# Optimization experiments

Hardware: AMD Instinct MI355X
Metric: run time of the kernel (lower is better)

## Reference

```python
import math
import jax, jax.numpy as jnp
import numpy as np

D_MODEL = 1024
HEADS = 16
D_K = D_MODEL // HEADS
BATCH = 4
SEQ = 2048


def setup_inputs() -> dict:
    key = jax.random.key(0)
    ks = jax.random.split(key, 7)
    q = jax.random.normal(ks[0], (BATCH, SEQ, D_MODEL), dtype=jnp.float32)
    k = jax.random.normal(ks[1], (BATCH, SEQ, D_MODEL), dtype=jnp.float32)
    v = jax.random.normal(ks[2], (BATCH, SEQ, D_MODEL), dtype=jnp.float32)
    # causal mask: True = masked (filled with -inf), broadcastable over batch & heads
    mask = jnp.triu(jnp.ones((SEQ, SEQ), dtype=bool), k=1)[None, None, :, :]
    s = 1.0 / math.sqrt(D_MODEL)
    Wq = jax.random.normal(ks[3], (D_MODEL, D_MODEL), dtype=jnp.float32) * s
    Wk = jax.random.normal(ks[4], (D_MODEL, D_MODEL), dtype=jnp.float32) * s
    Wv = jax.random.normal(ks[5], (D_MODEL, D_MODEL), dtype=jnp.float32) * s
    Wo = jax.random.normal(ks[6], (D_MODEL, D_MODEL), dtype=jnp.float32) * s
    return {"q": q, "k": k, "v": v, "mask": mask, "Wq": Wq, "Wk": Wk, "Wv": Wv, "Wo": Wo}


def reference(q, k, v, mask, Wq, Wk, Wv, Wo):
    B, S, _ = q.shape
    # Linear(d_model, d_model, bias=False): y = x @ W.T
    def proj(x, W):
        return (x @ W.T).reshape(B, S, HEADS, D_K).transpose(0, 2, 1, 3)  # [B,H,S,Dk]
    qh, kh, vh = proj(q, Wq), proj(k, Wk), proj(v, Wv)
    scores = jnp.einsum('bhqd,bhkd->bhqk', qh, kh) / math.sqrt(D_K)
    scores = jnp.where(mask, -jnp.inf, scores)
    attn = jax.nn.softmax(scores, axis=-1)  # dropout p=0 is identity
    ctx = jnp.einsum('bhqk,bhkd->bhqd', attn, vh)
    ctx = ctx.transpose(0, 2, 1, 3).reshape(B, S, D_MODEL)
    return ctx @ Wo.T
```

## Files before the change

kernel.cpp:

```cpp
#include <hip/hip_runtime.h>
#include <hip/hip_bf16.h>
#include <stdint.h>

#define S_LEN 2048
#define DMODEL 1024
#define HEADS 16
#define DK 64
#define LDK 72

#define QSCALE 0.18033688011112042f

typedef __attribute__((ext_vector_type(8))) short bf16x8;
typedef __attribute__((ext_vector_type(4))) float f32x4;

__device__ __forceinline__ unsigned short f2bf(float f) {
    union { float f; unsigned u; } c; c.f = f;
    unsigned u = c.u;
    u += 0x7fffu + ((u >> 16) & 1u);
    return (unsigned short)(u >> 16);
}

__device__ __forceinline__ unsigned pkbf(float a, float b) {
    union { float f; unsigned u; } ca, cb; ca.f = a; cb.f = b;
    unsigned ua = ca.u + (0x7fffu + ((ca.u >> 16) & 1u));
    unsigned ub = cb.u + (0x7fffu + ((cb.u >> 16) & 1u));
    return __builtin_amdgcn_perm(ub, ua, 0x07060302);
}

__device__ __forceinline__ unsigned cvtpk(float a, float b) {
    unsigned r;
    asm("v_cvt_pk_bf16_f32 %0, %1, %2" : "=v"(r) : "v"(a), "v"(b));
    return r;
}

__device__ __forceinline__ void g2lds16(const unsigned short* g, unsigned short* l) {
    __builtin_amdgcn_global_load_lds((const __attribute__((address_space(1))) void*)g,
                                     (__attribute__((address_space(3))) void*)l, 16, 0, 0);
}

__global__ __launch_bounds__(256) void convert_kernel(
    const float* __restrict__ q, const float* __restrict__ k, const float* __restrict__ v,
    const float* __restrict__ Wq, const float* __restrict__ Wk, const float* __restrict__ Wv,
    const float* __restrict__ Wo,
    unsigned short* __restrict__ qbf, unsigned short* __restrict__ kbf,
    unsigned short* __restrict__ vbf, unsigned short* __restrict__ wbf)
{
    const float* src; unsigned short* dst; int n8;
    const int y = blockIdx.y;
    if (y == 0)      { src = q;  dst = qbf;           n8 = 1048576; }
    else if (y == 1) { src = k;  dst = kbf;           n8 = 1048576; }
    else if (y == 2) { src = v;  dst = vbf;           n8 = 1048576; }
    else if (y == 3) { src = Wq; dst = wbf;           n8 = 131072; }
    else if (y == 4) { src = Wk; dst = wbf + 1048576; n8 = 131072; }
    else if (y == 5) { src = Wv; dst = wbf + 2097152; n8 = 131072; }
    else             { src = Wo; dst = wbf + 3145728; n8 = 131072; }
    int i = blockIdx.x * 256 + threadIdx.x;
    if (i >= n8) return;
    float4 f0 = ((const float4*)src)[(size_t)2 * i];
    float4 f1 = ((const float4*)src)[(size_t)2 * i + 1];
    union { unsigned u[4]; uint4 v; } o;
    o.u[0] = pkbf(f0.x, f0.y); o.u[1] = pkbf(f0.z, f0.w);
    o.u[2] = pkbf(f1.x, f1.y); o.u[3] = pkbf(f1.z, f1.w);
    *(uint4*)&dst[(size_t)8 * i] = o.v;
}

__device__ __forceinline__ void gemm_core_128x128(
    const unsigned short* __restrict__ Apanel,
    const unsigned short* __restrict__ Bpanel,
    unsigned short* sm,
    f32x4 acc[4][4])
{
    const int t    = threadIdx.x;
    const int lane = t & 63;
    const int w    = t >> 6;
    const int wm   = w >> 1;
    const int wn   = w & 1;
    const int lrow = lane & 15;
    const int quad = lane >> 4;

    const int l8   = lane >> 3;
    const int c16s = (lane & 7) ^ l8;
    const unsigned short* gA = Apanel + (size_t)(w * 8 + l8) * 1024 + c16s * 8;
    const unsigned short* gB = Bpanel + (size_t)(w * 8 + l8) * 1024 + c16s * 8;
    unsigned short* lA = sm + w * 512;
    unsigned short* lB = sm + 8192 + w * 512;

#define STAGE_KT(bufsel, kt) do {                                         \
        unsigned short* la = lA + (bufsel) * 16384;                       \
        unsigned short* lb = lB + (bufsel) * 16384;                       \
        const unsigned short* ga = gA + (kt) * 64;                        \
        const unsigned short* gb = gB + (kt) * 64;                        \
        g2lds16(ga,                       la);                            \
        g2lds16(ga + (size_t)32 * 1024,   la + 2048);                     \
        g2lds16(ga + (size_t)64 * 1024,   la + 4096);                     \
        g2lds16(ga + (size_t)96 * 1024,   la + 6144);                     \
        g2lds16(gb,                       lb);                            \
        g2lds16(gb + (size_t)32 * 1024,   lb + 2048);                     \
        g2lds16(gb + (size_t)64 * 1024,   lb + 4096);                     \
        g2lds16(gb + (size_t)96 * 1024,   lb + 6144);                     \
    } while (0)

    for (int i = 0; i < 4; i++) for (int j = 0; j < 4; j++) acc[i][j] = (f32x4){0.f, 0.f, 0.f, 0.f};

    STAGE_KT(0, 0);

#pragma unroll 1
    for (int kt = 0; kt < 16; ++kt) {
        const int buf = kt & 1;
        if (kt < 15) {
            STAGE_KT(buf ^ 1, kt + 1);
            asm volatile("s_waitcnt vmcnt(8)" ::: "memory");
        } else {
            asm volatile("s_waitcnt vmcnt(0)" ::: "memory");
        }
        __builtin_amdgcn_sched_barrier(0);
        __builtin_amdgcn_s_barrier();
        __builtin_amdgcn_sched_barrier(0);

        const unsigned short* tA = sm + buf * 16384;
        const unsigned short* tB = sm + buf * 16384 + 8192;
        for (int kh = 0; kh < 2; ++kh) {
            const int cs = ((kh * 4 + quad) ^ (lrow & 7)) * 8;
            bf16x8 a[4], b[4];
            for (int mi = 0; mi < 4; mi++)
                a[mi] = *(const bf16x8*)&tA[(wm * 64 + mi * 16 + lrow) * 64 + cs];
            for (int nj = 0; nj < 4; nj++)
                b[nj] = *(const bf16x8*)&tB[(wn * 64 + nj * 16 + lrow) * 64 + cs];
            __builtin_amdgcn_s_setprio(1);
            for (int mi = 0; mi < 4; mi++)
                for (int nj = 0; nj < 4; nj++)
                    acc[mi][nj] = __builtin_amdgcn_mfma_f32_16x16x32_bf16(a[mi], b[nj], acc[mi][nj], 0, 0, 0);
            __builtin_amdgcn_s_setprio(0);
        }
        __builtin_amdgcn_sched_barrier(0);
        __builtin_amdgcn_s_barrier();
        __builtin_amdgcn_sched_barrier(0);
    }
#undef STAGE_KT
}

__global__ __launch_bounds__(256, 2) void proj_gemm_kernel(
    const unsigned short* __restrict__ qbf, const unsigned short* __restrict__ kbf,
    const unsigned short* __restrict__ vbf, const unsigned short* __restrict__ wbf,
    unsigned short* __restrict__ qh, unsigned short* __restrict__ kh,
    unsigned short* __restrict__ vh_t)
{
    const int h   = (int)(blockIdx.x + 64 * (blockIdx.y + 8 * blockIdx.z));
    const int s   = h >> 3;
    const int panel = (h & 7) * 24 + (s >> 3);
    const int by  = s & 7;
    const int z   = panel >> 6;
    const int bx  = panel & 63;

    const unsigned short* A; const unsigned short* Bm; unsigned short* Y;
    if (z == 0)      { A = qbf; Bm = wbf;           Y = qh;   }
    else if (z == 1) { A = kbf; Bm = wbf + 1048576; Y = kh;   }
    else             { A = vbf; Bm = wbf + 2097152; Y = vh_t; }

    __shared__ unsigned short sm[32768];

    const int m0 = bx * 128;
    const int n0 = by * 128;

    f32x4 acc[4][4];
    gemm_core_128x128(A + (size_t)m0 * 1024, Bm + (size_t)n0 * 1024, sm, acc);

    const int t = threadIdx.x, lane = t & 63;
    const int wm = (t >> 6) >> 1, wn = (t >> 6) & 1;
    const int lrow = lane & 15, quad = lane >> 4;
    const float scale = (z == 0) ? QSCALE : 1.0f;
    for (int i = 0; i < 4; i++) {
        int grow = m0 + wm * 64 + i * 16 + quad * 4;
        for (int j = 0; j < 4; j++) {
            int gcol = n0 + wn * 64 + j * 16 + lrow;
            int hh = gcol >> 6, d = gcol & 63;
            for (int r = 0; r < 4; r++) {
                int row = grow + r;
                int b_ = row >> 11;
                int s_ = row & 2047;
                unsigned short val = f2bf(acc[i][j][r] * scale);
                if (z == 2)
                    Y[(((size_t)(b_ * HEADS + hh) * DK) + d) * S_LEN + s_] = val;
                else
                    Y[(((size_t)(b_ * HEADS + hh) * S_LEN) + s_) * DK + d] = val;
            }
        }
    }
}

__global__ __launch_bounds__(256, 2) void outproj_gemm_kernel(
    const unsigned short* __restrict__ ctx, const unsigned short* __restrict__ wobf,
    float* __restrict__ out)
{
    const int h   = (int)(blockIdx.x + 64 * blockIdx.y);
    const int s   = h >> 3;
    const int bx  = (h & 7) * 8 + (s >> 3);
    const int by  = s & 7;

    __shared__ unsigned short sm[32768];

    const int m0 = bx * 128;
    const int n0 = by * 128;

    f32x4 acc[4][4];
    gemm_core_128x128(ctx + (size_t)m0 * 1024, wobf + (size_t)n0 * 1024, sm, acc);

    const int t = threadIdx.x, lane = t & 63;
    const int wm = (t >> 6) >> 1, wn = (t >> 6) & 1;
    const int lrow = lane & 15, quad = lane >> 4;
    for (int i = 0; i < 4; i++) {
        int grow = m0 + wm * 64 + i * 16 + quad * 4;
        for (int j = 0; j < 4; j++) {
            int gcol = n0 + wn * 64 + j * 16 + lrow;
            for (int r = 0; r < 4; r++)
                out[(size_t)(grow + r) * DMODEL + gcol] = acc[i][j][r];
        }
    }
}

__global__ __launch_bounds__(256, 4) void attn_kernel(
    const unsigned short* __restrict__ qh, const unsigned short* __restrict__ kh,
    const unsigned short* __restrict__ vh_t, unsigned short* __restrict__ ctx)
{
    __shared__ unsigned short sK[64 * LDK];
    __shared__ unsigned short sVt[64 * LDK];
    __shared__ unsigned short sPT[4][16 * LDK];

    const int t    = threadIdx.x;
    const int lane = t & 63;
    const int wid  = t >> 6;
    const int lin  = (int)(blockIdx.y * gridDim.x + blockIdx.x);
    const int wlin = (lin & 7) * 128 + (lin >> 3);
    const int qx   = wlin & 15;
    const int bh   = wlin >> 4;
    const size_t base = (size_t)bh * S_LEN * DK;
    const int lrow = lane & 15;
    const int quad = lane >> 4;
    const int b_ = bh >> 4, h_ = bh & 15;
    unsigned short* myPT = &sPT[wid][0];

    const int sr0 = t >> 3;
    const int sc0 = (t & 7) * 8;
    const unsigned short* gK = kh + base;
    const unsigned short* gV = vh_t + base;

    for (int pass = 0; pass < 2; ++pass) {
        const int qt = pass ? (31 - qx) : qx;
        const int q0 = qt * 64;
        const int qw0 = q0 + wid * 16;

        bf16x8 qreg[2];
        for (int h = 0; h < 2; ++h)
            qreg[h] = *(const bf16x8*)&qh[base + (size_t)(qw0 + lrow) * DK + h * 32 + quad * 8];

        f32x4 o[4];
        for (int mf = 0; mf < 4; mf++) o[mf] = (f32x4){0.f, 0.f, 0.f, 0.f};
        float lstat = 0.f;

        const int ntiles = qt + 1;

        uint4 rK0 = *(const uint4*)&gK[(size_t)sr0 * DK + sc0];
        uint4 rK1 = *(const uint4*)&gK[(size_t)(sr0 + 32) * DK + sc0];
        uint4 rV0 = *(const uint4*)&gV[(size_t)sr0 * S_LEN + sc0];
        uint4 rV1 = *(const uint4*)&gV[(size_t)(sr0 + 32) * S_LEN + sc0];

        for (int kt = 0; kt < ntiles; ++kt) {
            const int k0 = kt * 64;
            __syncthreads();
            *(uint4*)&sK [sr0 * LDK + sc0]        = rK0;
            *(uint4*)&sK [(sr0 + 32) * LDK + sc0] = rK1;
            *(uint4*)&sVt[sr0 * LDK + sc0]        = rV0;
            *(uint4*)&sVt[(sr0 + 32) * LDK + sc0] = rV1;
            if (kt + 1 < ntiles) {
                const int kn = k0 + 64;
                rK0 = *(const uint4*)&gK[(size_t)(kn + sr0) * DK + sc0];
                rK1 = *(const uint4*)&gK[(size_t)(kn + sr0 + 32) * DK + sc0];
                rV0 = *(const uint4*)&gV[(size_t)sr0 * S_LEN + kn + sc0];
                rV1 = *(const uint4*)&gV[(size_t)(sr0 + 32) * S_LEN + kn + sc0];
            }
            __syncthreads();

            f32x4 st[4];
            for (int mf = 0; mf < 4; mf++) st[mf] = (f32x4){0.f, 0.f, 0.f, 0.f};
            for (int h = 0; h < 2; ++h) {
                bf16x8 kf[4];
                for (int mf = 0; mf < 4; mf++)
                    kf[mf] = *(const bf16x8*)&sK[(mf * 16 + lrow) * LDK + h * 32 + quad * 8];
                __builtin_amdgcn_s_setprio(1);
                for (int mf = 0; mf < 4; mf++)
                    st[mf] = __builtin_amdgcn_mfma_f32_16x16x32_bf16(kf[mf], qreg[h], st[mf], 0, 0, 0);
                __builtin_amdgcn_s_setprio(0);
            }

            if (kt == qt) {
                const int qidx = qw0 + lrow;
                for (int mf = 0; mf < 4; mf++)
                    for (int r = 0; r < 4; r++) {
                        int key = k0 + mf * 16 + quad * 4 + r;
                        if (key > qidx) st[mf][r] = -INFINITY;
                    }
            }

            {
                float rsum = 0.f;
                for (int mf = 0; mf < 4; mf++) {
                    float p0 = exp2f(st[mf][0]);
                    float p1 = exp2f(st[mf][1]);
                    float p2 = exp2f(st[mf][2]);
                    float p3 = exp2f(st[mf][3]);
                    rsum += (p0 + p1) + (p2 + p3);
                    uint2 pk;
                    pk.x = cvtpk(p0, p1);
                    pk.y = cvtpk(p2, p3);
                    *(uint2*)&myPT[lrow * LDK + mf * 16 + quad * 4] = pk;
                }
                lstat += rsum;
            }

            for (int h = 0; h < 2; ++h) {
                bf16x8 vf[4];
                for (int mf = 0; mf < 4; mf++)
                    vf[mf] = *(const bf16x8*)&sVt[(mf * 16 + lrow) * LDK + h * 32 + quad * 8];
                bf16x8 pf = *(const bf16x8*)&myPT[lrow * LDK + h * 32 + quad * 8];
                __builtin_amdgcn_s_setprio(1);
                for (int mf = 0; mf < 4; mf++)
                    o[mf] = __builtin_amdgcn_mfma_f32_16x16x32_bf16(vf[mf], pf, o[mf], 0, 0, 0);
                __builtin_amdgcn_s_setprio(0);
            }
        }

        {
            float ls = lstat;
            ls += __shfl_xor(ls, 16);
            ls += __shfl_xor(ls, 32);
            float inv = 1.f / ls;
            int s_ = qw0 + lrow;
            size_t rowbase = (((size_t)(b_ * S_LEN + s_)) * HEADS + h_) * DK;
            for (int mf = 0; mf < 4; mf++) {
                int d0 = mf * 16 + quad * 4;
                uint2 pk;
                pk.x = pkbf(o[mf][0] * inv, o[mf][1] * inv);
                pk.y = pkbf(o[mf][2] * inv, o[mf][3] * inv);
                *(uint2*)&ctx[rowbase + d0] = pk;
            }
        }
    }
}

__global__ __launch_bounds__(256) void proj_fb_kernel(
    const float* __restrict__ q, const float* __restrict__ k, const float* __restrict__ v,
    const float* __restrict__ Wq, const float* __restrict__ Wk, const float* __restrict__ Wv,
    unsigned short* __restrict__ qh, unsigned short* __restrict__ kh, unsigned short* __restrict__ vh_t)
{
    const float* X; const float* W; unsigned short* Y;
    if (blockIdx.z == 0)      { X = q; W = Wq; Y = qh; }
    else if (blockIdx.z == 1) { X = k; W = Wk; Y = kh; }
    else                      { X = v; W = Wv; Y = vh_t; }

    __shared__ short sA[128 * LDK];
    __shared__ short sB[128 * LDK];
    const int t = threadIdx.x, lane = t & 63, wid = t >> 6;
    const int wrow = (wid >> 1) * 64, wcol = (wid & 1) * 64;
    const int m0 = blockIdx.x * 128, n0 = blockIdx.y * 128;
    const int lrow = lane & 15, quad = lane >> 4, lk = quad * 8;

    f32x4 acc[4][4];
    for (int i = 0; i < 4; i++) for (int j = 0; j < 4; j++) acc[i][j] = (f32x4){0.f, 0.f, 0.f, 0.f};

    for (int kb = 0; kb < DMODEL; kb += 64) {
        for (int it = 0; it < 8; ++it) {
            int idx = t + it * 256;
            int row = idx >> 4, c4 = (idx & 15) * 4;
            float4 fa = *(const float4*)&X[(size_t)(m0 + row) * DMODEL + kb + c4];
            float4 fb = *(const float4*)&W[(size_t)(n0 + row) * DMODEL + kb + c4];
            short4 sa = { (short)f2bf(fa.x), (short)f2bf(fa.y), (short)f2bf(fa.z), (short)f2bf(fa.w) };
            short4 sb = { (short)f2bf(fb.x), (short)f2bf(fb.y), (short)f2bf(fb.z), (short)f2bf(fb.w) };
            *(short4*)&sA[row * LDK + c4] = sa;
            *(short4*)&sB[row * LDK + c4] = sb;
        }
        __syncthreads();
        for (int kk = 0; kk < 64; kk += 32) {
            bf16x8 a[4], b[4];
            for (int i = 0; i < 4; i++) a[i] = *(const bf16x8*)&sA[(wrow + i * 16 + lrow) * LDK + kk + lk];
            for (int j = 0; j < 4; j++) b[j] = *(const bf16x8*)&sB[(wcol + j * 16 + lrow) * LDK + kk + lk];
            for (int i = 0; i < 4; i++)
                for (int j = 0; j < 4; j++)
                    acc[i][j] = __builtin_amdgcn_mfma_f32_16x16x32_bf16(a[i], b[j], acc[i][j], 0, 0, 0);
        }
        __syncthreads();
    }

    const float scale = (blockIdx.z == 0) ? QSCALE : 1.0f;
    for (int i = 0; i < 4; i++) {
        int grow = m0 + wrow + i * 16 + quad * 4;
        for (int j = 0; j < 4; j++) {
            int gcol = n0 + wcol + j * 16 + lrow;
            int h = gcol >> 6, d = gcol & 63;
            for (int r = 0; r < 4; r++) {
                int row = grow + r, b_ = row >> 11, s_ = row & 2047;
                unsigned short val = f2bf(acc[i][j][r] * scale);
                if (blockIdx.z == 2)
                    Y[(((size_t)(b_ * HEADS + h) * DK) + d) * S_LEN + s_] = val;
                else
                    Y[(((size_t)(b_ * HEADS + h) * S_LEN) + s_) * DK + d] = val;
            }
        }
    }
}

__global__ __launch_bounds__(256) void outproj_fb_kernel(
    const unsigned short* __restrict__ ctx, const float* __restrict__ Wo, float* __restrict__ out)
{
    __shared__ short sA[128 * LDK];
    __shared__ short sB[128 * LDK];
    const int t = threadIdx.x, lane = t & 63, wid = t >> 6;
    const int wrow = (wid >> 1) * 64, wcol = (wid & 1) * 64;
    const int m0 = blockIdx.x * 128, n0 = blockIdx.y * 128;
    const int lrow = lane & 15, quad = lane >> 4, lk = quad * 8;

    f32x4 acc[4][4];
    for (int i = 0; i < 4; i++) for (int j = 0; j < 4; j++) acc[i][j] = (f32x4){0.f, 0.f, 0.f, 0.f};

    for (int kb = 0; kb < DMODEL; kb += 64) {
        for (int it = 0; it < 4; ++it) {
            int idx = t + it * 256;
            int row = idx >> 3, c8 = (idx & 7) * 8;
            *(uint4*)&sA[row * LDK + c8] = *(const uint4*)&ctx[(size_t)(m0 + row) * DMODEL + kb + c8];
        }
        for (int it = 0; it < 8; ++it) {
            int idx = t + it * 256;
            int row = idx >> 4, c4 = (idx & 15) * 4;
            float4 fb = *(const float4*)&Wo[(size_t)(n0 + row) * DMODEL + kb + c4];
            short4 sb = { (short)f2bf(fb.x), (short)f2bf(fb.y), (short)f2bf(fb.z), (short)f2bf(fb.w) };
            *(short4*)&sB[row * LDK + c4] = sb;
        }
        __syncthreads();
        for (int kk = 0; kk < 64; kk += 32) {
            bf16x8 a[4], b[4];
            for (int i = 0; i < 4; i++) a[i] = *(const bf16x8*)&sA[(wrow + i * 16 + lrow) * LDK + kk + lk];
            for (int j = 0; j < 4; j++) b[j] = *(const bf16x8*)&sB[(wcol + j * 16 + lrow) * LDK + kk + lk];
            for (int i = 0; i < 4; i++)
                for (int j = 0; j < 4; j++)
                    acc[i][j] = __builtin_amdgcn_mfma_f32_16x16x32_bf16(a[i], b[j], acc[i][j], 0, 0, 0);
        }
        __syncthreads();
    }

    for (int i = 0; i < 4; i++) {
        int grow = m0 + wrow + i * 16 + quad * 4;
        for (int j = 0; j < 4; j++) {
            int gcol = n0 + wcol + j * 16 + lrow;
            for (int r = 0; r < 4; r++)
                out[(size_t)(grow + r) * DMODEL + gcol] = acc[i][j][r];
        }
    }
}

extern "C" void kernel_launch(void* const* d_in, const int* in_sizes, int n_in,
                              void* d_out, int out_size, void* d_ws, size_t ws_size,
                              hipStream_t stream)
{
    const float* q  = (const float*)d_in[0];
    const float* k  = (const float*)d_in[1];
    const float* v  = (const float*)d_in[2];
    const float* Wq = (const float*)d_in[4];
    const float* Wk = (const float*)d_in[5];
    const float* Wv = (const float*)d_in[6];
    const float* Wo = (const float*)d_in[7];
    float* out = (float*)d_out;

    const size_t M8 = (size_t)8 * 1024 * 1024;
    const size_t need = (size_t)(52) * 1024 * 1024 * 2;

    if (ws_size >= need) {
        unsigned short* qbf  = (unsigned short*)d_ws;
        unsigned short* kbf  = qbf + M8;
        unsigned short* vbf  = kbf + M8;
        unsigned short* wbf  = vbf + M8;
        unsigned short* qh   = wbf + (size_t)4 * 1024 * 1024;
        unsigned short* kh   = qh + M8;
        unsigned short* vh_t = kh + M8;
        unsigned short* ctx  = qbf;

        dim3 gCvt(4096, 7);
        convert_kernel<<<gCvt, 256, 0, stream>>>(q, k, v, Wq, Wk, Wv, Wo, qbf, kbf, vbf, wbf);

        dim3 gProj(64, 8, 3);
        proj_gemm_kernel<<<gProj, 256, 0, stream>>>(qbf, kbf, vbf, wbf, qh, kh, vh_t);

        dim3 gAttn(16, 64);
        attn_kernel<<<gAttn, 256, 0, stream>>>(qh, kh, vh_t, ctx);

        dim3 gOut(64, 8);
        outproj_gemm_kernel<<<gOut, 256, 0, stream>>>(ctx, wbf + (size_t)3 * 1024 * 1024, out);
    } else {
        unsigned short* qh   = (unsigned short*)d_ws;
        unsigned short* kh   = qh + M8;
        unsigned short* vh_t = kh + M8;
        unsigned short* ctx  = vh_t + M8;

        dim3 gProj(64, 8, 3);
        proj_fb_kernel<<<gProj, 256, 0, stream>>>(q, k, v, Wq, Wk, Wv, qh, kh, vh_t);

        dim3 gAttn(16, 64);
        attn_kernel<<<gAttn, 256, 0, stream>>>(qh, kh, vh_t, ctx);

        dim3 gOut(64, 8);
        outproj_fb_kernel<<<gOut, 256, 0, stream>>>(ctx, Wo, out);
    }
}
```

Before: 329.0 us.

## Store GEMM operands in tiled 128x64 blocked layout for contiguous panel loads

The bf16 conversion kernel and the attention ctx writer now emit operands in a blocked layout where each 128-row by 64-column k-tile is contiguous. The GEMM core then loads each k-step from one contiguous 16 KB block instead of 128 rows strided by 1024 elements, and the fallback out-projection reads ctx with the same layout. This aims to improve DRAM/TLB locality and reduce address arithmetic for the staged global-to-LDS loads. Every producer and consumer of these buffers has to agree on the layout, so a missed fallback path would produce wrong results.

Measured after the change: 339.1 us. 3.1% more time.

```diff
diff --git a/kernel.cpp b/kernel.cpp
--- a/kernel.cpp
+++ b/kernel.cpp
@@ -9,6 +9,7 @@
 #define LDK 72
 
 #define QSCALE 0.18033688011112042f
+
 
 typedef __attribute__((ext_vector_type(8))) short bf16x8;
 typedef __attribute__((ext_vector_type(4))) float f32x4;
@@ -61,7 +62,10 @@
     union { unsigned u[4]; uint4 v; } o;
     o.u[0] = pkbf(f0.x, f0.y); o.u[1] = pkbf(f0.z, f0.w);
     o.u[2] = pkbf(f1.x, f1.y); o.u[3] = pkbf(f1.z, f1.w);
-    *(uint4*)&dst[(size_t)8 * i] = o.v;
+    const int m  = i >> 7;
+    const int k8 = (i & 127) * 8;
+    const size_t didx = ((size_t)((m >> 7) * 16 + (k8 >> 6)) * 128 + (m & 127)) * 64 + (k8 & 63);
+    *(uint4*)&dst[didx] = o.v;
 }
 
 __device__ __forceinline__ void gemm_core_128x128(
@@ -80,24 +84,24 @@
 
     const int l8   = lane >> 3;
     const int c16s = (lane & 7) ^ l8;
-    const unsigned short* gA = Apanel + (size_t)(w * 8 + l8) * 1024 + c16s * 8;
-    const unsigned short* gB = Bpanel + (size_t)(w * 8 + l8) * 1024 + c16s * 8;
+    const unsigned short* gA = Apanel + (w * 8 + l8) * 64 + c16s * 8;
+    const unsigned short* gB = Bpanel + (w * 8 + l8) * 64 + c16s * 8;
     unsigned short* lA = sm + w * 512;
     unsigned short* lB = sm + 8192 + w * 512;
 
 #define STAGE_KT(bufsel, kt) do {                                         \
         unsigned short* la = lA + (bufsel) * 16384;                       \
         unsigned short* lb = lB + (bufsel) * 16384;                       \
-        const unsigned short* ga = gA + (kt) * 64;                        \
-        const unsigned short* gb = gB + (kt) * 64;                        \
-        g2lds16(ga,                       la);                            \
-        g2lds16(ga + (size_t)32 * 1024,   la + 2048);                     \
-        g2lds16(ga + (size_t)64 * 1024,   la + 4096);                     \
-        g2lds16(ga + (size_t)96 * 1024,   la + 6144);                     \
-        g2lds16(gb,                       lb);                            \
-        g2lds16(gb + (size_t)32 * 1024,   lb + 2048);                     \
-        g2lds16(gb + (size_t)64 * 1024,   lb + 4096);                     \
-        g2lds16(gb + (size_t)96 * 1024,   lb + 6144);                     \
+        const unsigned short* ga = gA + (size_t)(kt) * 8192;              \
+        const unsigned short* gb = gB + (size_t)(kt) * 8192;              \
+        g2lds16(ga,        la);                                           \
+        g2lds16(ga + 2048, la + 2048);                                    \
+        g2lds16(ga + 4096, la + 4096);                                    \
+        g2lds16(ga + 6144, la + 6144);                                    \
+        g2lds16(gb,        lb);                                           \
+        g2lds16(gb + 2048, lb + 2048);                                    \
+        g2lds16(gb + 4096, lb + 4096);                                    \
+        g2lds16(gb + 6144, lb + 6144);                                    \
     } while (0)
 
     for (int i = 0; i < 4; i++) for (int j = 0; j < 4; j++) acc[i][j] = (f32x4){0.f, 0.f, 0.f, 0.f};
@@ -163,7 +167,7 @@
     const int n0 = by * 128;
 
     f32x4 acc[4][4];
-    gemm_core_128x128(A + (size_t)m0 * 1024, Bm + (size_t)n0 * 1024, sm, acc);
+    gemm_core_128x128(A + (size_t)bx * 131072, Bm + (size_t)by * 131072, sm, acc);
 
     const int t = threadIdx.x, lane = t & 63;
     const int wm = (t >> 6) >> 1, wn = (t >> 6) & 1;
@@ -203,7 +207,7 @@
     const int n0 = by * 128;
 
     f32x4 acc[4][4];
-    gemm_core_128x128(ctx + (size_t)m0 * 1024, wobf + (size_t)n0 * 1024, sm, acc);
+    gemm_core_128x128(ctx + (size_t)bx * 131072, wobf + (size_t)by * 131072, sm, acc);
 
     const int t = threadIdx.x, lane = t & 63;
     const int wm = (t >> 6) >> 1, wn = (t >> 6) & 1;
@@ -335,13 +339,14 @@
             ls += __shfl_xor(ls, 32);
             float inv = 1.f / ls;
             int s_ = qw0 + lrow;
-            size_t rowbase = (((size_t)(b_ * S_LEN + s_)) * HEADS + h_) * DK;
+            int grow = b_ * S_LEN + s_;
+            size_t tb = ((size_t)((grow >> 7) * 16 + h_) * 128 + (grow & 127)) * 64;
             for (int mf = 0; mf < 4; mf++) {
                 int d0 = mf * 16 + quad * 4;
                 uint2 pk;
                 pk.x = pkbf(o[mf][0] * inv, o[mf][1] * inv);
                 pk.y = pkbf(o[mf][2] * inv, o[mf][3] * inv);
-                *(uint2*)&ctx[rowbase + d0] = pk;
+                *(uint2*)&ctx[tb + d0] = pk;
             }
         }
     }
@@ -422,10 +427,11 @@
     for (int i = 0; i < 4; i++) for (int j = 0; j < 4; j++) acc[i][j] = (f32x4){0.f, 0.f, 0.f, 0.f};
 
     for (int kb = 0; kb < DMODEL; kb += 64) {
+        const size_t tbase = ((size_t)(blockIdx.x * 16 + (kb >> 6))) * 8192;
         for (int it = 0; it < 4; ++it) {
             int idx = t + it * 256;
             int row = idx >> 3, c8 = (idx & 7) * 8;
-            *(uint4*)&sA[row * LDK + c8] = *(const uint4*)&ctx[(size_t)(m0 + row) * DMODEL + kb + c8];
+            *(uint4*)&sA[row * LDK + c8] = *(const uint4*)&ctx[tbase + (size_t)row * 64 + c8];
         }
         for (int it = 0; it < 8; ++it) {
             int idx = t + it * 256;
```

## Split GEMM k-tile into four quadrant phases interleaving LDS reads, loads and MFMAs

Applied to the files above, without the earlier changes.

Restructures the shared 128x128 GEMM core so each k-tile is computed in four 2x2 sub-block phases. The next tile's global-to-LDS loads are spread across those phases in quarters, so loads overlap with the MFMA work instead of being issued all at once. The launch bounds drop the minimum of two blocks per CU, which gives the compiler more registers but may lower occupancy. The change adds many more workgroup barriers per k-tile and relies on careful vmcnt accounting for correctness.

Measured after the change: 333.9 us. Within noise of the previous version (+1.5%).

```diff
diff --git a/kernel.cpp b/kernel.cpp
--- a/kernel.cpp
+++ b/kernel.cpp
@@ -85,61 +85,124 @@
     unsigned short* lA = sm + w * 512;
     unsigned short* lB = sm + 8192 + w * 512;
 
-#define STAGE_KT(bufsel, kt) do {                                         \
-        unsigned short* la = lA + (bufsel) * 16384;                       \
-        unsigned short* lb = lB + (bufsel) * 16384;                       \
-        const unsigned short* ga = gA + (kt) * 64;                        \
-        const unsigned short* gb = gB + (kt) * 64;                        \
-        g2lds16(ga,                       la);                            \
-        g2lds16(ga + (size_t)32 * 1024,   la + 2048);                     \
-        g2lds16(ga + (size_t)64 * 1024,   la + 4096);                     \
-        g2lds16(ga + (size_t)96 * 1024,   la + 6144);                     \
-        g2lds16(gb,                       lb);                            \
-        g2lds16(gb + (size_t)32 * 1024,   lb + 2048);                     \
-        g2lds16(gb + (size_t)64 * 1024,   lb + 4096);                     \
-        g2lds16(gb + (size_t)96 * 1024,   lb + 6144);                     \
+#define STAGE_A_LO(bufsel, kt) do {                                        \
+        unsigned short* la = lA + (bufsel) * 16384;                        \
+        const unsigned short* ga = gA + (kt) * 64;                         \
+        g2lds16(ga,                       la);                             \
+        g2lds16(ga + (size_t)32 * 1024,   la + 2048);                      \
     } while (0)
+#define STAGE_A_HI(bufsel, kt) do {                                        \
+        unsigned short* la = lA + (bufsel) * 16384;                        \
+        const unsigned short* ga = gA + (kt) * 64;                         \
+        g2lds16(ga + (size_t)64 * 1024,   la + 4096);                      \
+        g2lds16(ga + (size_t)96 * 1024,   la + 6144);                      \
+    } while (0)
+#define STAGE_B_LO(bufsel, kt) do {                                        \
+        unsigned short* lb = lB + (bufsel) * 16384;                        \
+        const unsigned short* gb = gB + (kt) * 64;                         \
+        g2lds16(gb,                       lb);                             \
+        g2lds16(gb + (size_t)32 * 1024,   lb + 2048);                      \
+    } while (0)
+#define STAGE_B_HI(bufsel, kt) do {                                        \
+        unsigned short* lb = lB + (bufsel) * 16384;                        \
+        const unsigned short* gb = gB + (kt) * 64;                         \
+        g2lds16(gb + (size_t)64 * 1024,   lb + 4096);                      \
+        g2lds16(gb + (size_t)96 * 1024,   lb + 6144);                      \
+    } while (0)
 
     for (int i = 0; i < 4; i++) for (int j = 0; j < 4; j++) acc[i][j] = (f32x4){0.f, 0.f, 0.f, 0.f};
 
-    STAGE_KT(0, 0);
+    STAGE_A_LO(0, 0); STAGE_A_HI(0, 0); STAGE_B_LO(0, 0); STAGE_B_HI(0, 0);
+    STAGE_A_LO(1, 1);
+    asm volatile("s_waitcnt vmcnt(2)" ::: "memory");
+    __builtin_amdgcn_sched_barrier(0);
+    __builtin_amdgcn_s_barrier();
+    __builtin_amdgcn_sched_barrier(0);
 
 #pragma unroll 1
     for (int kt = 0; kt < 16; ++kt) {
         const int buf = kt & 1;
-        if (kt < 15) {
-            STAGE_KT(buf ^ 1, kt + 1);
-            asm volatile("s_waitcnt vmcnt(8)" ::: "memory");
+        const unsigned short* tA = sm + buf * 16384;
+        const unsigned short* tB = sm + buf * 16384 + 8192;
+        const bool more = (kt + 1 < 16);
+        bf16x8 al[2][2], ah[2][2], bl[2][2], bh[2][2];
+
+        for (int kh = 0; kh < 2; ++kh) {
+            const int cs = ((kh * 4 + quad) ^ (lrow & 7)) * 8;
+            for (int mi = 0; mi < 2; mi++) al[mi][kh] = *(const bf16x8*)&tA[(wm * 64 + mi * 16 + lrow) * 64 + cs];
+            for (int nj = 0; nj < 2; nj++) bl[nj][kh] = *(const bf16x8*)&tB[(wn * 64 + nj * 16 + lrow) * 64 + cs];
+        }
+        if (more) STAGE_A_HI(buf ^ 1, kt + 1);
+        __builtin_amdgcn_s_barrier();
+        __builtin_amdgcn_sched_barrier(0);
+        __builtin_amdgcn_s_setprio(1);
+        for (int kh = 0; kh < 2; ++kh)
+            for (int mi = 0; mi < 2; mi++)
+                for (int nj = 0; nj < 2; nj++)
+                    acc[mi][nj] = __builtin_amdgcn_mfma_f32_16x16x32_bf16(al[mi][kh], bl[nj][kh], acc[mi][nj], 0, 0, 0);
+        __builtin_amdgcn_s_setprio(0);
+        __builtin_amdgcn_s_barrier();
+        __builtin_amdgcn_sched_barrier(0);
+
+        for (int kh = 0; kh < 2; ++kh) {
+            const int cs = ((kh * 4 + quad) ^ (lrow & 7)) * 8;
+            for (int nj = 0; nj < 2; nj++) bh[nj][kh] = *(const bf16x8*)&tB[(wn * 64 + (2 + nj) * 16 + lrow) * 64 + cs];
+        }
+        if (more) STAGE_B_LO(buf ^ 1, kt + 1);
+        __builtin_amdgcn_s_barrier();
+        __builtin_amdgcn_sched_barrier(0);
+        __builtin_amdgcn_s_setprio(1);
+        for (int kh = 0; kh < 2; ++kh)
+            for (int mi = 0; mi < 2; mi++)
+                for (int nj = 0; nj < 2; nj++)
+                    acc[mi][2 + nj] = __builtin_amdgcn_mfma_f32_16x16x32_bf16(al[mi][kh], bh[nj][kh], acc[mi][2 + nj], 0, 0, 0);
+        __builtin_amdgcn_s_setprio(0);
+        __builtin_amdgcn_s_barrier();
+        __builtin_amdgcn_sched_barrier(0);
+
+        for (int kh = 0; kh < 2; ++kh) {
+            const int cs = ((kh * 4 + quad) ^ (lrow & 7)) * 8;
+            for (int mi = 0; mi < 2; mi++) ah[mi][kh] = *(const bf16x8*)&tA[(wm * 64 + (2 + mi) * 16 + lrow) * 64 + cs];
+        }
+        if (more) STAGE_B_HI(buf ^ 1, kt + 1);
+        __builtin_amdgcn_s_barrier();
+        __builtin_amdgcn_sched_barrier(0);
+        __builtin_amdgcn_s_setprio(1);
+        for (int kh = 0; kh < 2; ++kh)
+            for (int mi = 0; mi < 2; mi++)
+                for (int nj = 0; nj < 2; nj++)
+                    acc[2 + mi][nj] = __builtin_amdgcn_mfma_f32_16x16x32_bf16(ah[mi][kh], bl[nj][kh], acc[2 + mi][nj], 0, 0, 0);
+        __builtin_amdgcn_s_setprio(0);
+        __builtin_amdgcn_s_barrier();
+        __builtin_amdgcn_sched_barrier(0);
+
+        __builtin_amdgcn_s_setprio(1);
+        for (int kh = 0; kh < 2; ++kh)
+            for (int mi = 0; mi < 2; mi++)
+                for (int nj = 0; nj < 2; nj++)
+                    acc[2 + mi][2 + nj] = __builtin_amdgcn_mfma_f32_16x16x32_bf16(ah[mi][kh], bh[nj][kh], acc[2 + mi][2 + nj], 0, 0, 0);
+        __builtin_amdgcn_s_setprio(0);
+
+        __builtin_amdgcn_sched_barrier(0);
+        __builtin_amdgcn_s_barrier();
+        __builtin_amdgcn_sched_barrier(0);
+        if (kt + 2 < 16) {
+            STAGE_A_LO(buf, kt + 2);
+            asm volatile("s_waitcnt vmcnt(2)" ::: "memory");
         } else {
             asm volatile("s_waitcnt vmcnt(0)" ::: "memory");
         }
         __builtin_amdgcn_sched_barrier(0);
         __builtin_amdgcn_s_barrier();
         __builtin_amdgcn_sched_barrier(0);
-
-        const unsigned short* tA = sm + buf * 16384;
-        const unsigned short* tB = sm + buf * 16384 + 8192;
-        for (int kh = 0; kh < 2; ++kh) {
-            const int cs = ((kh * 4 + quad) ^ (lrow & 7)) * 8;
-            bf16x8 a[4], b[4];
-            for (int mi = 0; mi < 4; mi++)
-                a[mi] = *(const bf16x8*)&tA[(wm * 64 + mi * 16 + lrow) * 64 + cs];
-            for (int nj = 0; nj < 4; nj++)
-                b[nj] = *(const bf16x8*)&tB[(wn * 64 + nj * 16 + lrow) * 64 + cs];
-            __builtin_amdgcn_s_setprio(1);
-            for (int mi = 0; mi < 4; mi++)
-                for (int nj = 0; nj < 4; nj++)
-                    acc[mi][nj] = __builtin_amdgcn_mfma_f32_16x16x32_bf16(a[mi], b[nj], acc[mi][nj], 0, 0, 0);
-            __builtin_amdgcn_s_setprio(0);
-        }
-        __builtin_amdgcn_sched_barrier(0);
-        __builtin_amdgcn_s_barrier();
-        __builtin_amdgcn_sched_barrier(0);
-    }
-#undef STAGE_KT
-}
-
-__global__ __launch_bounds__(256, 2) void proj_gemm_kernel(
+    }
+#undef STAGE_A_LO
+#undef STAGE_A_HI
+#undef STAGE_B_LO
+#undef STAGE_B_HI
+}
+
+__global__ __launch_bounds__(256) void proj_gemm_kernel(
     const unsigned short* __restrict__ qbf, const unsigned short* __restrict__ kbf,
     const unsigned short* __restrict__ vbf, const unsigned short* __restrict__ wbf,
     unsigned short* __restrict__ qh, unsigned short* __restrict__ kh,
@@ -188,7 +251,7 @@
     }
 }
 
-__global__ __launch_bounds__(256, 2) void outproj_gemm_kernel(
+__global__ __launch_bounds__(256) void outproj_gemm_kernel(
     const unsigned short* __restrict__ ctx, const unsigned short* __restrict__ wobf,
     float* __restrict__ out)
 {
```

## Load GEMM A operand directly into registers, staging only B through LDS

Applied to the files above, without the earlier changes.

The shared 128x128 GEMM core now reads the A panel straight from global memory into registers (double-buffered as even/odd register sets) and stages only the B panel through LDS, halving the shared-memory footprint. The main loop is unrolled by two K tiles with explicit vmcnt waits and barriers. Launch bounds drop the minimum of two blocks per CU. The aim is to cut LDS traffic and LDS capacity pressure. The cost is more VGPRs and uncoalesced per-lane 16-byte global loads for A that are no longer shared between waves with the same wm.

New measurement: 410.8 us. 1.25x slower.

```diff
diff --git a/kernel.cpp b/kernel.cpp
--- a/kernel.cpp
+++ b/kernel.cpp
@@ -80,66 +80,95 @@
 
     const int l8   = lane >> 3;
     const int c16s = (lane & 7) ^ l8;
-    const unsigned short* gA = Apanel + (size_t)(w * 8 + l8) * 1024 + c16s * 8;
     const unsigned short* gB = Bpanel + (size_t)(w * 8 + l8) * 1024 + c16s * 8;
-    unsigned short* lA = sm + w * 512;
-    unsigned short* lB = sm + 8192 + w * 512;
-
-#define STAGE_KT(bufsel, kt) do {                                         \
-        unsigned short* la = lA + (bufsel) * 16384;                       \
-        unsigned short* lb = lB + (bufsel) * 16384;                       \
-        const unsigned short* ga = gA + (kt) * 64;                        \
-        const unsigned short* gb = gB + (kt) * 64;                        \
-        g2lds16(ga,                       la);                            \
-        g2lds16(ga + (size_t)32 * 1024,   la + 2048);                     \
-        g2lds16(ga + (size_t)64 * 1024,   la + 4096);                     \
-        g2lds16(ga + (size_t)96 * 1024,   la + 6144);                     \
-        g2lds16(gb,                       lb);                            \
-        g2lds16(gb + (size_t)32 * 1024,   lb + 2048);                     \
-        g2lds16(gb + (size_t)64 * 1024,   lb + 4096);                     \
-        g2lds16(gb + (size_t)96 * 1024,   lb + 6144);                     \
+
+    const unsigned short* gAr = Apanel + (size_t)(wm * 64 + lrow) * 1024 + quad * 8;
+
+#define STAGE_B(bufsel, kt) do {                                           \
+        unsigned short* lb = sm + (bufsel) * 8192 + w * 512;               \
+        const unsigned short* gb = gB + (size_t)(kt) * 64;                 \
+        g2lds16(gb,                       lb);                             \
+        g2lds16(gb + (size_t)32 * 1024,   lb + 2048);                      \
+        g2lds16(gb + (size_t)64 * 1024,   lb + 4096);                      \
+        g2lds16(gb + (size_t)96 * 1024,   lb + 6144);                      \
     } while (0)
 
+#define LOAD_A(dst, kt) do {                                               \
+        _Pragma("unroll")                                                  \
+        for (int mi = 0; mi < 4; mi++)                                     \
+            _Pragma("unroll")                                              \
+            for (int kh = 0; kh < 2; kh++)                                 \
+                dst[mi * 2 + kh] = *(const bf16x8*)&gAr[(size_t)mi * 16384 \
+                                     + (size_t)(kt) * 64 + kh * 32];       \
+    } while (0)
+
+#define COMPUTE_TILE(areg, bufsel) do {                                    \
+        const unsigned short* tB = sm + (bufsel) * 8192;                   \
+        bf16x8 bfr[4][2];                                                  \
+        _Pragma("unroll")                                                  \
+        for (int kh = 0; kh < 2; kh++) {                                   \
+            const int cs = ((kh * 4 + quad) ^ (lrow & 7)) * 8;             \
+            _Pragma("unroll")                                              \
+            for (int nj = 0; nj < 4; nj++)                                 \
+                bfr[nj][kh] = *(const bf16x8*)&tB[(wn * 64 + nj * 16 + lrow) * 64 + cs]; \
+        }                                                                  \
+        __builtin_amdgcn_s_setprio(1);                                     \
+        _Pragma("unroll")                                                  \
+        for (int kh = 0; kh < 2; kh++)                                     \
+            _Pragma("unroll")                                              \
+            for (int mi = 0; mi < 4; mi++)                                 \
+                _Pragma("unroll")                                          \
+                for (int nj = 0; nj < 4; nj++)                             \
+                    acc[mi][nj] = __builtin_amdgcn_mfma_f32_16x16x32_bf16( \
+                        areg[mi * 2 + kh], bfr[nj][kh], acc[mi][nj], 0, 0, 0); \
+        __builtin_amdgcn_s_setprio(0);                                     \
+    } while (0)
+
     for (int i = 0; i < 4; i++) for (int j = 0; j < 4; j++) acc[i][j] = (f32x4){0.f, 0.f, 0.f, 0.f};
 
-    STAGE_KT(0, 0);
+    bf16x8 aE[8], aO[8];
+
+    LOAD_A(aE, 0);
+    STAGE_B(0, 0);
 
 #pragma unroll 1
-    for (int kt = 0; kt < 16; ++kt) {
-        const int buf = kt & 1;
-        if (kt < 15) {
-            STAGE_KT(buf ^ 1, kt + 1);
-            asm volatile("s_waitcnt vmcnt(8)" ::: "memory");
+    for (int i = 0; i < 8; ++i) {
+        const int e = 2 * i;
+        LOAD_A(aO, e + 1);
+        STAGE_B(1, e + 1);
+        __builtin_amdgcn_sched_barrier(0);
+        asm volatile("s_waitcnt vmcnt(12)" ::: "memory");
+        __builtin_amdgcn_sched_barrier(0);
+        __builtin_amdgcn_s_barrier();
+        __builtin_amdgcn_sched_barrier(0);
+        COMPUTE_TILE(aE, 0);
+        __builtin_amdgcn_sched_barrier(0);
+        __builtin_amdgcn_s_barrier();
+        __builtin_amdgcn_sched_barrier(0);
+
+        if (e + 2 < 16) {
+            LOAD_A(aE, e + 2);
+            STAGE_B(0, e + 2);
+            __builtin_amdgcn_sched_barrier(0);
+            asm volatile("s_waitcnt vmcnt(12)" ::: "memory");
         } else {
+            __builtin_amdgcn_sched_barrier(0);
             asm volatile("s_waitcnt vmcnt(0)" ::: "memory");
         }
         __builtin_amdgcn_sched_barrier(0);
         __builtin_amdgcn_s_barrier();
         __builtin_amdgcn_sched_barrier(0);
-
-        const unsigned short* tA = sm + buf * 16384;
-        const unsigned short* tB = sm + buf * 16384 + 8192;
-        for (int kh = 0; kh < 2; ++kh) {
-            const int cs = ((kh * 4 + quad) ^ (lrow & 7)) * 8;
-            bf16x8 a[4], b[4];
-            for (int mi = 0; mi < 4; mi++)
-                a[mi] = *(const bf16x8*)&tA[(wm * 64 + mi * 16 + lrow) * 64 + cs];
-            for (int nj = 0; nj < 4; nj++)
-                b[nj] = *(const bf16x8*)&tB[(wn * 64 + nj * 16 + lrow) * 64 + cs];
-            __builtin_amdgcn_s_setprio(1);
-            for (int mi = 0; mi < 4; mi++)
-                for (int nj = 0; nj < 4; nj++)
-                    acc[mi][nj] = __builtin_amdgcn_mfma_f32_16x16x32_bf16(a[mi], b[nj], acc[mi][nj], 0, 0, 0);
-            __builtin_amdgcn_s_setprio(0);
-        }
+        COMPUTE_TILE(aO, 1);
         __builtin_amdgcn_sched_barrier(0);
         __builtin_amdgcn_s_barrier();
         __builtin_amdgcn_sched_barrier(0);
     }
-#undef STAGE_KT
-}
-
-__global__ __launch_bounds__(256, 2) void proj_gemm_kernel(
+#undef STAGE_B
+#undef LOAD_A
+#undef COMPUTE_TILE
+}
+
+__global__ __launch_bounds__(256) void proj_gemm_kernel(
     const unsigned short* __restrict__ qbf, const unsigned short* __restrict__ kbf,
     const unsigned short* __restrict__ vbf, const unsigned short* __restrict__ wbf,
     unsigned short* __restrict__ qh, unsigned short* __restrict__ kh,
@@ -157,7 +186,7 @@
     else if (z == 1) { A = kbf; Bm = wbf + 1048576; Y = kh;   }
     else             { A = vbf; Bm = wbf + 2097152; Y = vh_t; }
 
-    __shared__ unsigned short sm[32768];
+    __shared__ unsigned short sm[16384];
 
     const int m0 = bx * 128;
     const int n0 = by * 128;
@@ -188,7 +217,7 @@
     }
 }
 
-__global__ __launch_bounds__(256, 2) void outproj_gemm_kernel(
+__global__ __launch_bounds__(256) void outproj_gemm_kernel(
     const unsigned short* __restrict__ ctx, const unsigned short* __restrict__ wobf,
     float* __restrict__ out)
 {
@@ -197,7 +226,7 @@
     const int bx  = (h & 7) * 8 + (s >> 3);
     const int by  = s & 7;
 
-    __shared__ unsigned short sm[32768];
+    __shared__ unsigned short sm[16384];
 
     const int m0 = bx * 128;
     const int n0 = by * 128;
```
